# Optimization experiments

Hardware: AMD Instinct MI355X
Metric: run time of the kernel (lower is better)

## Reference

```python
import jax, jax.numpy as jnp
import numpy as np

B, S, NI, NQK, NV = 8, 2048, 1024, 128, 128

def setup_inputs() -> dict:
    key = jax.random.key(0)
    ks = jax.random.split(key, 7)
    sc_i = 1.0 / np.sqrt(NI)
    x = jax.random.normal(ks[0], (B, S, NI), dtype=jnp.float32)
    Wq = jax.random.uniform(ks[1], (NQK, NI), dtype=jnp.float32, minval=-sc_i, maxval=sc_i)
    bq = jax.random.uniform(ks[2], (NQK,), dtype=jnp.float32, minval=-sc_i, maxval=sc_i)
    Wk = jax.random.uniform(ks[3], (NQK, NI), dtype=jnp.float32, minval=-sc_i, maxval=sc_i)
    bk = jax.random.uniform(ks[4], (NQK,), dtype=jnp.float32, minval=-sc_i, maxval=sc_i)
    Wv = jax.random.uniform(ks[5], (NV, NI), dtype=jnp.float32, minval=-sc_i, maxval=sc_i)
    bv = jax.random.uniform(ks[6], (NV,), dtype=jnp.float32, minval=-sc_i, maxval=sc_i)
    return {"x": x, "Wq": Wq, "bq": bq, "Wk": Wk, "bk": bk, "Wv": Wv, "bv": bv}

def reference(x, Wq, bq, Wk, bk, Wv, bv):
    # torch nn.Linear: y = x @ W.T + b
    q = jnp.einsum('bsi,di->bsd', x, Wq) + bq  # [B,S,NQK]
    k = jnp.einsum('bsi,di->bsd', x, Wk) + bk  # [B,S,NQK]
    v = jnp.einsum('bsi,di->bsd', x, Wv) + bv  # [B,S,NV]
    # NOTE: original has no 1/sqrt(d) scaling
    Z = jnp.einsum('bqd,bkd->bqk', q, k)       # [B,S,S]
    Z = jax.nn.softmax(Z, axis=2)
    y = jnp.einsum('bqk,bkd->bqd', Z, v)       # [B,S,NV]
    return y
```

## Files before the change

kernel.cpp:

```cpp
#include <hip/hip_runtime.h>
#include <hip/hip_bf16.h>
#include <cstdint>

#define B_ 8
#define S_ 2048
#define NI_ 1024
#define D_ 128
#define M_ (B_ * S_)

typedef __attribute__((ext_vector_type(8))) short bf16x8;
typedef __attribute__((ext_vector_type(8))) unsigned short u16x8;
typedef __attribute__((ext_vector_type(4))) float f32x4;

__device__ __forceinline__ unsigned short f2bf(float f) {
    union { float f; uint32_t u; } v; v.f = f;
    uint32_t u = v.u;
    u += 0x7fff + ((u >> 16) & 1);
    return (unsigned short)(u >> 16);
}

__device__ __forceinline__ void gload16(const void* g, void* l) {
    __builtin_amdgcn_global_load_lds((const __attribute__((address_space(1))) void*)g,
                                     (__attribute__((address_space(3))) void*)l, 16, 0, 0);
}

__global__ __launch_bounds__(256) void k_pack_w(const float* __restrict__ Wq, const float* __restrict__ bq,
                                                const float* __restrict__ Wk, const float* __restrict__ bk,
                                                const float* __restrict__ Wv, const float* __restrict__ bv,
                                                unsigned short* __restrict__ wb, float* __restrict__ bias) {
    int t = blockIdx.x * 256 + threadIdx.x;
    int e = t * 8;
    const float* src; int off;
    if (e < 131072)      { src = Wq; off = e; }
    else if (e < 262144) { src = Wk; off = e - 131072; }
    else                 { src = Wv; off = e - 262144; }
    float4 a = *(const float4*)(src + off);
    float4 b = *(const float4*)(src + off + 4);
    u16x8 r;
    r[0] = f2bf(a.x); r[1] = f2bf(a.y); r[2] = f2bf(a.z); r[3] = f2bf(a.w);
    r[4] = f2bf(b.x); r[5] = f2bf(b.y); r[6] = f2bf(b.z); r[7] = f2bf(b.w);
    *(u16x8*)(wb + e) = r;
    if (t < 384)
        bias[t] = (t < 128) ? bq[t] : (t < 256) ? bk[t - 128] : bv[t - 256];
}

__global__ __launch_bounds__(256) void k_qkv(const float* __restrict__ x,
                                             const unsigned short* __restrict__ wb,
                                             const float* __restrict__ bias,
                                             unsigned short* __restrict__ q,
                                             unsigned short* __restrict__ kout,
                                             unsigned short* __restrict__ vT) {
    __shared__ __align__(16) unsigned short As[2][128 * 32];
    __shared__ __align__(16) unsigned short Bs[2][128 * 32];
    const int tid = threadIdx.x;
    const int m0 = blockIdx.x * 128;
    const int n0 = blockIdx.y * 128;
    const int l = tid & 63, w = tid >> 6;
    const int wr = w >> 1, wc = w & 1;
    const int lr = l & 15, lg = l >> 4;
    const int sr = tid >> 2;
    const int sc = (tid & 3) * 8;

    f32x4 acc[4][4] = {};
    float4 a0, a1, a2, a3;

#define LOADA(k0off) do { \
    const float* xg0 = x + (long)(m0 + sr) * NI_ + (k0off) + sc; \
    const float* xg1 = x + (long)(m0 + 64 + sr) * NI_ + (k0off) + sc; \
    a0 = *(const float4*)xg0; a1 = *(const float4*)(xg0 + 4); \
    a2 = *(const float4*)xg1; a3 = *(const float4*)(xg1 + 4); } while (0)

#define CVTWRITEA(buf) do { \
    union { __hip_bfloat162 h[4]; u16x8 v; } r0, r1; \
    r0.h[0] = __float22bfloat162_rn(make_float2(a0.x, a0.y)); \
    r0.h[1] = __float22bfloat162_rn(make_float2(a0.z, a0.w)); \
    r0.h[2] = __float22bfloat162_rn(make_float2(a1.x, a1.y)); \
    r0.h[3] = __float22bfloat162_rn(make_float2(a1.z, a1.w)); \
    r1.h[0] = __float22bfloat162_rn(make_float2(a2.x, a2.y)); \
    r1.h[1] = __float22bfloat162_rn(make_float2(a2.z, a2.w)); \
    r1.h[2] = __float22bfloat162_rn(make_float2(a3.x, a3.y)); \
    r1.h[3] = __float22bfloat162_rn(make_float2(a3.z, a3.w)); \
    *(u16x8*)((unsigned short*)As[buf] + tid * 8) = r0.v; \
    *(u16x8*)((unsigned short*)As[buf] + 2048 + tid * 8) = r1.v; } while (0)

    LOADA(0);
    gload16(wb + (long)(n0 + sr) * NI_ + sc,      (unsigned short*)Bs[0] + tid * 8);
    gload16(wb + (long)(n0 + 64 + sr) * NI_ + sc, (unsigned short*)Bs[0] + 2048 + tid * 8);
    CVTWRITEA(0);
    __syncthreads();

    int cur = 0;
    for (int k0 = 0; k0 < NI_; k0 += 32) {
        bool more = (k0 + 32 < NI_);
        if (more) {
            gload16(wb + (long)(n0 + sr) * NI_ + k0 + 32 + sc,      (unsigned short*)Bs[cur ^ 1] + tid * 8);
            gload16(wb + (long)(n0 + 64 + sr) * NI_ + k0 + 32 + sc, (unsigned short*)Bs[cur ^ 1] + 2048 + tid * 8);
            LOADA(k0 + 32);
        }

        bf16x8 a[4], b[4];
#pragma unroll
        for (int i = 0; i < 4; i++)
            a[i] = *(const bf16x8*)((unsigned short*)As[cur] + (wr * 64 + i * 16 + lr) * 32 + lg * 8);
#pragma unroll
        for (int j = 0; j < 4; j++)
            b[j] = *(const bf16x8*)((unsigned short*)Bs[cur] + (wc * 64 + j * 16 + lr) * 32 + lg * 8);
#pragma unroll
        for (int i = 0; i < 4; i++)
#pragma unroll
            for (int j = 0; j < 4; j++)
                acc[i][j] = __builtin_amdgcn_mfma_f32_16x16x32_bf16(a[i], b[j], acc[i][j], 0, 0, 0);

        if (more) CVTWRITEA(cur ^ 1);
        __syncthreads();
        cur ^= 1;
    }
#undef LOADA
#undef CVTWRITEA

#pragma unroll
    for (int i = 0; i < 4; i++)
#pragma unroll
        for (int j = 0; j < 4; j++)
#pragma unroll
            for (int r = 0; r < 4; r++) {
                int row = m0 + wr * 64 + i * 16 + lg * 4 + r;
                int n = n0 + wc * 64 + j * 16 + lr;
                float val = acc[i][j][r] + bias[n];
                unsigned short bv16 = f2bf(val);
                if (n0 == 0)        q[(long)row * 128 + n] = bv16;
                else if (n0 == 128) kout[(long)row * 128 + (n - 128)] = bv16;
                else {
                    int bb = row >> 11, s = row & 2047, d = n - 256;
                    vT[((long)bb * 128 + d) * (long)S_ + s] = bv16;
                }
            }
}

#define SHIFT_ 16.0f
__global__ __launch_bounds__(256, 2) void k_attn(const unsigned short* __restrict__ q,
                                                 const unsigned short* __restrict__ kk,
                                                 const unsigned short* __restrict__ vT,
                                                 float* __restrict__ o_part,
                                                 float* __restrict__ L_part) {
    __shared__ __align__(16) unsigned short Kl[2 * 64 * 128];
    __shared__ __align__(16) unsigned short Vl[2 * 128 * 64];
    __shared__ __align__(16) unsigned short Plds[4 * 32 * 64];
    const int tid = threadIdx.x, l = tid & 63, w = tid >> 6;
    const int b = blockIdx.z, ks = blockIdx.y;
    const int q0 = blockIdx.x * 128 + w * 32;
    const int lr = l & 15, lg = l >> 4;
    const unsigned short* qB = q  + (long)b * S_ * 128;
    const unsigned short* kB = kk + (long)b * S_ * 128;
    const unsigned short* vB = vT + (long)b * 128 * S_;
    char* Pw = (char*)Plds + w * 4096;
    const int kv_base = ks * 512;
    const int lsw = (lr & 7) << 4;

    const int krow = tid >> 2, kcb = (tid & 3) * 64;
    const int vrow = tid >> 1, vcb = (tid & 1) * 64;
    const int kswz = (krow & 7) << 4, vswz = (vrow & 7) << 4;

    bf16x8 qf[2][4];
#pragma unroll
    for (int a = 0; a < 2; a++)
#pragma unroll
        for (int kc = 0; kc < 4; kc++)
            qf[a][kc] = *(const bf16x8*)(qB + (long)(q0 + a * 16 + lr) * 128 + kc * 32 + lg * 8);

    {
        const unsigned short* kg = kB + (long)(kv_base + krow) * 128 + (tid & 3) * 32;
        const unsigned short* vg = vB + (long)vrow * S_ + kv_base + (tid & 1) * 32;
        u16x8 k0v = *(const u16x8*)(kg),      k1v = *(const u16x8*)(kg + 8);
        u16x8 k2v = *(const u16x8*)(kg + 16), k3v = *(const u16x8*)(kg + 24);
        u16x8 v0v = *(const u16x8*)(vg),      v1v = *(const u16x8*)(vg + 8);
        u16x8 v2v = *(const u16x8*)(vg + 16), v3v = *(const u16x8*)(vg + 24);
        char* kd = (char*)Kl; char* vd = (char*)Vl;
        *(u16x8*)(kd + ((krow * 256 + kcb)      ^ kswz)) = k0v;
        *(u16x8*)(kd + ((krow * 256 + kcb + 16) ^ kswz)) = k1v;
        *(u16x8*)(kd + ((krow * 256 + kcb + 32) ^ kswz)) = k2v;
        *(u16x8*)(kd + ((krow * 256 + kcb + 48) ^ kswz)) = k3v;
        *(u16x8*)(vd + ((vrow * 128 + vcb)      ^ vswz)) = v0v;
        *(u16x8*)(vd + ((vrow * 128 + vcb + 16) ^ vswz)) = v1v;
        *(u16x8*)(vd + ((vrow * 128 + vcb + 32) ^ vswz)) = v2v;
        *(u16x8*)(vd + ((vrow * 128 + vcb + 48) ^ vswz)) = v3v;
    }
    __syncthreads();

    float psum[2][4] = {};
    f32x4 o[2][8] = {};
    int cur = 0;

    for (int t = 0; t < 8; t++) {
        u16x8 k0v, k1v, k2v, k3v, v0v, v1v, v2v, v3v;
        if (t < 7) {
            int kv = kv_base + (t + 1) * 64;
            const unsigned short* kg = kB + (long)(kv + krow) * 128 + (tid & 3) * 32;
            const unsigned short* vg = vB + (long)vrow * S_ + kv + (tid & 1) * 32;
            k0v = *(const u16x8*)(kg);      k1v = *(const u16x8*)(kg + 8);
            k2v = *(const u16x8*)(kg + 16); k3v = *(const u16x8*)(kg + 24);
            v0v = *(const u16x8*)(vg);      v1v = *(const u16x8*)(vg + 8);
            v2v = *(const u16x8*)(vg + 16); v3v = *(const u16x8*)(vg + 24);
        }

        const char* kd = (const char*)Kl + cur * 16384;
        const char* vd = (const char*)Vl + cur * 16384;

        f32x4 sa[2][4] = {};
#pragma unroll
        for (int j = 0; j < 4; j++) {
            bf16x8 kf[4];
#pragma unroll
            for (int kc = 0; kc < 4; kc++)
                kf[kc] = *(const bf16x8*)(kd + (((j * 16 + lr) * 256 + kc * 64 + lg * 16) ^ lsw));
#pragma unroll
            for (int a = 0; a < 2; a++)
#pragma unroll
                for (int kc = 0; kc < 4; kc++)
                    sa[a][j] = __builtin_amdgcn_mfma_f32_16x16x32_bf16(qf[a][kc], kf[kc], sa[a][j], 0, 0, 0);
        }

#pragma unroll
        for (int a = 0; a < 2; a++)
#pragma unroll
            for (int r = 0; r < 4; r++) {
                int row = a * 16 + lg * 4 + r;
#pragma unroll
                for (int j = 0; j < 4; j++) {
                    float pj = __expf(sa[a][j][r] - SHIFT_);
                    psum[a][r] += pj;
                    int bo = (row * 128 + (j * 16 + lr) * 2) ^ ((row & 7) << 4);
                    *(unsigned short*)(Pw + bo) = f2bf(pj);
                }
            }

        bf16x8 pa[2][2];
#pragma unroll
        for (int a = 0; a < 2; a++) {
            pa[a][0] = *(const bf16x8*)(Pw + (((a * 16 + lr) * 128 + lg * 16) ^ lsw));
            pa[a][1] = *(const bf16x8*)(Pw + (((a * 16 + lr) * 128 + 64 + lg * 16) ^ lsw));
        }

#pragma unroll
        for (int c = 0; c < 8; c++) {
            int dr = c * 16 + lr;
            bf16x8 vf0 = *(const bf16x8*)(vd + ((dr * 128 + lg * 16) ^ lsw));
            bf16x8 vf1 = *(const bf16x8*)(vd + ((dr * 128 + 64 + lg * 16) ^ lsw));
#pragma unroll
            for (int a = 0; a < 2; a++) {
                o[a][c] = __builtin_amdgcn_mfma_f32_16x16x32_bf16(pa[a][0], vf0, o[a][c], 0, 0, 0);
                o[a][c] = __builtin_amdgcn_mfma_f32_16x16x32_bf16(pa[a][1], vf1, o[a][c], 0, 0, 0);
            }
        }

        if (t < 7) {
            char* kdn = (char*)Kl + (cur ^ 1) * 16384;
            char* vdn = (char*)Vl + (cur ^ 1) * 16384;
            *(u16x8*)(kdn + ((krow * 256 + kcb)      ^ kswz)) = k0v;
            *(u16x8*)(kdn + ((krow * 256 + kcb + 16) ^ kswz)) = k1v;
            *(u16x8*)(kdn + ((krow * 256 + kcb + 32) ^ kswz)) = k2v;
            *(u16x8*)(kdn + ((krow * 256 + kcb + 48) ^ kswz)) = k3v;
            *(u16x8*)(vdn + ((vrow * 128 + vcb)      ^ vswz)) = v0v;
            *(u16x8*)(vdn + ((vrow * 128 + vcb + 16) ^ vswz)) = v1v;
            *(u16x8*)(vdn + ((vrow * 128 + vcb + 32) ^ vswz)) = v2v;
            *(u16x8*)(vdn + ((vrow * 128 + vcb + 48) ^ vswz)) = v3v;
        }
        __syncthreads();
        cur ^= 1;
    }

#pragma unroll
    for (int a = 0; a < 2; a++)
#pragma unroll
        for (int r = 0; r < 4; r++) {
            float ps = psum[a][r];
            ps += __shfl_xor(ps, 1);
            ps += __shfl_xor(ps, 2);
            ps += __shfl_xor(ps, 4);
            ps += __shfl_xor(ps, 8);
            if (lr == 0)
                L_part[((long)ks * B_ + b) * S_ + q0 + a * 16 + lg * 4 + r] = ps;
        }
#pragma unroll
    for (int a = 0; a < 2; a++)
#pragma unroll
        for (int c = 0; c < 8; c++)
#pragma unroll
            for (int r = 0; r < 4; r++) {
                int row = q0 + a * 16 + lg * 4 + r, col = c * 16 + lr;
                o_part[(((long)ks * B_ + b) * S_ + row) * 128 + col] = o[a][c][r];
            }
}

__global__ __launch_bounds__(256) void k_comb(const float* __restrict__ op,
                                              const float* __restrict__ Lp,
                                              float* __restrict__ out) {
    int t = blockIdx.x * 256 + threadIdx.x;
    int row = t >> 5;
    int c4 = (t & 31) * 4;
    float ax = 0.f, ay = 0.f, az = 0.f, aw = 0.f, Ls = 0.f;
#pragma unroll
    for (int ts = 0; ts < 4; ts++) {
        float4 v = *(const float4*)(op + (((long)ts * M_ + row) << 7) + c4);
        ax += v.x; ay += v.y; az += v.z; aw += v.w;
        Ls += Lp[(long)ts * M_ + row];
    }
    float inv = 1.f / Ls;
    float4 r; r.x = ax * inv; r.y = ay * inv; r.z = az * inv; r.w = aw * inv;
    *(float4*)(out + ((long)row << 7) + c4) = r;
}

extern "C" void kernel_launch(void* const* d_in, const int* in_sizes, int n_in,
                              void* d_out, int out_size, void* d_ws, size_t ws_size,
                              hipStream_t stream) {
    const float* x  = (const float*)d_in[0];
    const float* Wq = (const float*)d_in[1];
    const float* bq = (const float*)d_in[2];
    const float* Wk = (const float*)d_in[3];
    const float* bk = (const float*)d_in[4];
    const float* Wv = (const float*)d_in[5];
    const float* bv = (const float*)d_in[6];
    float* out = (float*)d_out;

    char* ws = (char*)d_ws;
    unsigned short* wb   = (unsigned short*)(ws + 33554432);
    float*          bias = (float*)(ws + 33554432 + 786432);
    unsigned short* qb   = (unsigned short*)(ws + 34344960);
    unsigned short* kb   = (unsigned short*)(ws + 38539264);
    unsigned short* vT   = (unsigned short*)(ws + 42733568);
    float* o_part = (float*)(ws);
    float* L_part = (float*)(ws + 46927872);

    k_pack_w<<<192, 256, 0, stream>>>(Wq, bq, Wk, bk, Wv, bv, wb, bias);
    k_qkv<<<dim3(128, 3), 256, 0, stream>>>(x, wb, bias, qb, kb, vT);
    k_attn<<<dim3(16, 4, 8), 256, 0, stream>>>(qb, kb, vT, o_part, L_part);
    k_comb<<<2048, 256, 0, stream>>>(o_part, L_part, out);
}
```

Before: 85.36 us.

## Retile QKV projection GEMM to 64x128 blocks with K=64 steps and swizzled LDS

The QKV projection kernel now uses 64-row M tiles instead of 128, doubling the grid to 768 blocks for better CU coverage. The K step grows from 32 to 64, halving loop iterations and barriers. LDS rows are XOR-swizzled to cut bank conflicts on the MFMA operand reads. In exchange, each weight tile is reused across fewer rows of x, so weight traffic per output rises, and each block does less work.

```diff
diff --git a/kernel.cpp b/kernel.cpp
--- a/kernel.cpp
+++ b/kernel.cpp
@@ -50,25 +50,38 @@
                                              unsigned short* __restrict__ q,
                                              unsigned short* __restrict__ kout,
                                              unsigned short* __restrict__ vT) {
-    __shared__ __align__(16) unsigned short As[2][128 * 32];
-    __shared__ __align__(16) unsigned short Bs[2][128 * 32];
+    __shared__ __align__(16) unsigned short As[2][64 * 64];
+    __shared__ __align__(16) unsigned short Bs[2][128 * 64];
     const int tid = threadIdx.x;
-    const int m0 = blockIdx.x * 128;
+    const int m0 = blockIdx.x * 64;
     const int n0 = blockIdx.y * 128;
     const int l = tid & 63, w = tid >> 6;
     const int wr = w >> 1, wc = w & 1;
     const int lr = l & 15, lg = l >> 4;
-    const int sr = tid >> 2;
-    const int sc = (tid & 3) * 8;
-
-    f32x4 acc[4][4] = {};
+    const int lsw = (lr & 7) << 4;
+
+    const int brow = tid >> 3;
+    const int sB = ((tid & 7) * 8) ^ (((tid >> 3) & 7) << 3);
+
+    const int arow = tid >> 2;
+    const int acol = (tid & 3) * 16;
+    const int amsk = (arow & 7) << 3;
+    const int adst0 = arow * 64 + (acol ^ amsk);
+    const int adst1 = arow * 64 + ((acol + 8) ^ amsk);
+
+    f32x4 acc[2][4] = {};
     float4 a0, a1, a2, a3;
 
 #define LOADA(k0off) do { \
-    const float* xg0 = x + (long)(m0 + sr) * NI_ + (k0off) + sc; \
-    const float* xg1 = x + (long)(m0 + 64 + sr) * NI_ + (k0off) + sc; \
-    a0 = *(const float4*)xg0; a1 = *(const float4*)(xg0 + 4); \
-    a2 = *(const float4*)xg1; a3 = *(const float4*)(xg1 + 4); } while (0)
+    const float* xg = x + (long)(m0 + arow) * NI_ + (k0off) + acol; \
+    a0 = *(const float4*)xg;        a1 = *(const float4*)(xg + 4); \
+    a2 = *(const float4*)(xg + 8);  a3 = *(const float4*)(xg + 12); } while (0)
+
+#define GLOADB(buf, k0off) do { \
+    _Pragma("unroll") \
+    for (int c = 0; c < 4; c++) \
+        gload16(wb + (long)(n0 + c * 32 + brow) * NI_ + (k0off) + sB, \
+                (unsigned short*)Bs[buf] + c * 2048 + tid * 8); } while (0)
 
 #define CVTWRITEA(buf) do { \
     union { __hip_bfloat162 h[4]; u16x8 v; } r0, r1; \
@@ -80,51 +93,60 @@
     r1.h[1] = __float22bfloat162_rn(make_float2(a2.z, a2.w)); \
     r1.h[2] = __float22bfloat162_rn(make_float2(a3.x, a3.y)); \
     r1.h[3] = __float22bfloat162_rn(make_float2(a3.z, a3.w)); \
-    *(u16x8*)((unsigned short*)As[buf] + tid * 8) = r0.v; \
-    *(u16x8*)((unsigned short*)As[buf] + 2048 + tid * 8) = r1.v; } while (0)
+    *(u16x8*)((unsigned short*)As[buf] + adst0) = r0.v; \
+    *(u16x8*)((unsigned short*)As[buf] + adst1) = r1.v; } while (0)
 
     LOADA(0);
-    gload16(wb + (long)(n0 + sr) * NI_ + sc,      (unsigned short*)Bs[0] + tid * 8);
-    gload16(wb + (long)(n0 + 64 + sr) * NI_ + sc, (unsigned short*)Bs[0] + 2048 + tid * 8);
+    GLOADB(0, 0);
     CVTWRITEA(0);
     __syncthreads();
 
     int cur = 0;
-    for (int k0 = 0; k0 < NI_; k0 += 32) {
-        bool more = (k0 + 32 < NI_);
+    for (int k0 = 0; k0 < NI_; k0 += 64) {
+        bool more = (k0 + 64 < NI_);
         if (more) {
-            gload16(wb + (long)(n0 + sr) * NI_ + k0 + 32 + sc,      (unsigned short*)Bs[cur ^ 1] + tid * 8);
-            gload16(wb + (long)(n0 + 64 + sr) * NI_ + k0 + 32 + sc, (unsigned short*)Bs[cur ^ 1] + 2048 + tid * 8);
-            LOADA(k0 + 32);
-        }
-
-        bf16x8 a[4], b[4];
-#pragma unroll
-        for (int i = 0; i < 4; i++)
-            a[i] = *(const bf16x8*)((unsigned short*)As[cur] + (wr * 64 + i * 16 + lr) * 32 + lg * 8);
+            GLOADB(cur ^ 1, k0 + 64);
+            LOADA(k0 + 64);
+        }
+
+        const char* ad = (const char*)As[cur];
+        const char* bd = (const char*)Bs[cur];
+        bf16x8 a[2][2], b[4][2];
+#pragma unroll
+        for (int i = 0; i < 2; i++)
+#pragma unroll
+            for (int kc = 0; kc < 2; kc++)
+                a[i][kc] = *(const bf16x8*)(ad + (wr * 32 + i * 16 + lr) * 128
+                                               + ((kc * 64 + lg * 16) ^ lsw));
 #pragma unroll
         for (int j = 0; j < 4; j++)
-            b[j] = *(const bf16x8*)((unsigned short*)Bs[cur] + (wc * 64 + j * 16 + lr) * 32 + lg * 8);
-#pragma unroll
-        for (int i = 0; i < 4; i++)
-#pragma unroll
-            for (int j = 0; j < 4; j++)
-                acc[i][j] = __builtin_amdgcn_mfma_f32_16x16x32_bf16(a[i], b[j], acc[i][j], 0, 0, 0);
+#pragma unroll
+            for (int kc = 0; kc < 2; kc++)
+                b[j][kc] = *(const bf16x8*)(bd + (wc * 64 + j * 16 + lr) * 128
+                                               + ((kc * 64 + lg * 16) ^ lsw));
+#pragma unroll
+        for (int kc = 0; kc < 2; kc++)
+#pragma unroll
+            for (int i = 0; i < 2; i++)
+#pragma unroll
+                for (int j = 0; j < 4; j++)
+                    acc[i][j] = __builtin_amdgcn_mfma_f32_16x16x32_bf16(a[i][kc], b[j][kc], acc[i][j], 0, 0, 0);
 
         if (more) CVTWRITEA(cur ^ 1);
         __syncthreads();
         cur ^= 1;
     }
 #undef LOADA
+#undef GLOADB
 #undef CVTWRITEA
 
 #pragma unroll
-    for (int i = 0; i < 4; i++)
+    for (int i = 0; i < 2; i++)
 #pragma unroll
         for (int j = 0; j < 4; j++)
 #pragma unroll
             for (int r = 0; r < 4; r++) {
-                int row = m0 + wr * 64 + i * 16 + lg * 4 + r;
+                int row = m0 + wr * 32 + i * 16 + lg * 4 + r;
                 int n = n0 + wc * 64 + j * 16 + lr;
                 float val = acc[i][j][r] + bias[n];
                 unsigned short bv16 = f2bf(val);
@@ -332,7 +354,7 @@
     float* L_part = (float*)(ws + 46927872);
 
     k_pack_w<<<192, 256, 0, stream>>>(Wq, bq, Wk, bk, Wv, bv, wb, bias);
-    k_qkv<<<dim3(128, 3), 256, 0, stream>>>(x, wb, bias, qb, kb, vT);
+    k_qkv<<<dim3(256, 3), 256, 0, stream>>>(x, wb, bias, qb, kb, vT);
     k_attn<<<dim3(16, 4, 8), 256, 0, stream>>>(qb, kb, vT, o_part, L_part);
     k_comb<<<2048, 256, 0, stream>>>(o_part, L_part, out);
 }
```

New measurement: 79.44 us. 1.07x faster.
